# Performance work log

Hardware: AMD Instinct MI355X
Metric: run time of the kernel (lower is better)

Reference implementation:

```python
import jax, jax.numpy as jnp
import numpy as np

KS = 3           # deformable kernel size
N = KS * KS      # 9 sampling points
PAD = 1
STRIDE = 1


def conv2d(x, w, b=None, stride=1, padding=0):
    out = jax.lax.conv_general_dilated(
        x, w, (stride, stride), [(padding, padding), (padding, padding)],
        dimension_numbers=("NCHW", "OIHW", "NCHW"))
    if b is not None:
        out = out + b[None, :, None, None]
    return out


def setup_inputs() -> dict:
    key = jax.random.key(0)
    k0, k1, k2, k3 = jax.random.split(key, 4)
    B, C, H, W, OUTC = 2, 64, 128, 128, 64
    x = jax.random.normal(k0, (B, C, H, W), jnp.float32)
    # p_conv: Conv2d(C, 2*N, 3, padding=1); small weights so offsets are O(1)
    Wp = jax.random.normal(k1, (2 * N, C, 3, 3), jnp.float32) * 0.01
    bp = jax.random.normal(k2, (2 * N,), jnp.float32) * 0.1
    # final conv: Conv2d(C, OUTC, ks, stride=ks, bias=None) -> no bias
    Wc = jax.random.normal(k3, (OUTC, C, KS, KS), jnp.float32) / np.sqrt(C * KS * KS)
    return {"x": x, "Wp": Wp, "bp": bp, "Wc": Wc}


def _gather(x_pad, qx, qy):
    # x_pad: [b,c,Hp,Wp]; qx,qy: [b,h,w,N] int32 -> [b,c,h,w,N]
    b, c, Hp, Wpd = x_pad.shape
    _, h, w, n = qx.shape
    idx = (qx * Wpd + qy).reshape(b, 1, h * w * n)
    xf = x_pad.reshape(b, c, Hp * Wpd)
    g = jnp.take_along_axis(xf, jnp.broadcast_to(idx, (b, c, h * w * n)), axis=2)
    return g.reshape(b, c, h, w, n)


def reference(x, Wp, bp, Wc):
    b, c, h, w = x.shape
    dt = x.dtype
    offset = conv2d(x, Wp, bp, stride=STRIDE, padding=1)  # [b,2N,h,w]
    x_pad = jnp.pad(x, ((0, 0), (0, 0), (PAD, PAD), (PAD, PAD)))
    Hp, Wpd = x_pad.shape[2], x_pad.shape[3]

    # kernel-relative offsets p_n (x part first, then y part; n = kx*KS + ky)
    rng = jnp.arange(-(KS - 1) // 2, (KS - 1) // 2 + 1, dtype=dt)
    pnx, pny = jnp.meshgrid(rng, rng, indexing="ij")
    # base grid p_0 (starts at 1 because of the zero padding)
    p0x = jnp.arange(1, h * STRIDE + 1, STRIDE, dtype=dt)
    p0y = jnp.arange(1, w * STRIDE + 1, STRIDE, dtype=dt)

    # sampling locations, split into x/y coords: [b,h,w,N]
    px = offset[:, :N].transpose(0, 2, 3, 1) + pnx.ravel() + p0x[None, :, None, None]
    py = offset[:, N:].transpose(0, 2, 3, 1) + pny.ravel() + p0y[None, None, :, None]

    qltx = jnp.clip(jnp.floor(px), 0, Hp - 1).astype(jnp.int32)
    qlty = jnp.clip(jnp.floor(py), 0, Wpd - 1).astype(jnp.int32)
    qrbx = jnp.clip(jnp.floor(px) + 1, 0, Hp - 1).astype(jnp.int32)
    qrby = jnp.clip(jnp.floor(py) + 1, 0, Wpd - 1).astype(jnp.int32)

    px = jnp.clip(px, 0, Hp - 1)
    py = jnp.clip(py, 0, Wpd - 1)

    # bilinear weights
    g_lt = (1 + (qltx - px)) * (1 + (qlty - py))
    g_rb = (1 - (qrbx - px)) * (1 - (qrby - py))
    g_lb = (1 + (qltx - px)) * (1 - (qrby - py))
    g_rt = (1 - (qrbx - px)) * (1 + (qlty - py))

    x_lt = _gather(x_pad, qltx, qlty)
    x_rb = _gather(x_pad, qrbx, qrby)
    x_lb = _gather(x_pad, qltx, qrby)
    x_rt = _gather(x_pad, qrbx, qlty)

    x_off = (g_lt[:, None] * x_lt + g_rb[:, None] * x_rb
             + g_lb[:, None] * x_lb + g_rt[:, None] * x_rt)  # [b,c,h,w,N]

    # unfold N=(kx,ky) into spatial: [b,c,h*KS,w*KS]
    x_off = x_off.reshape(b, c, h, w, KS, KS).transpose(0, 1, 2, 4, 3, 5)
    x_off = x_off.reshape(b, c, h * KS, w * KS)

    return conv2d(x_off, Wc, None, stride=KS, padding=0)  # [b,outc,h,w]
```

## Files before the change

### kernel.cpp

```cpp
#include <hip/hip_runtime.h>
#include <hip/hip_bf16.h>

#define BB 2
#define CC 64
#define HH 128
#define WW 128
#define OC 64
#define HW (HH * WW)

typedef __attribute__((ext_vector_type(8))) short bf16x8;
typedef __attribute__((ext_vector_type(4))) float f32x4;

__device__ __forceinline__ unsigned short bfbits(float f) {
    __hip_bfloat16 h = __float2bfloat16(f);
    return __builtin_bit_cast(unsigned short, h);
}
__device__ __forceinline__ float frombits(unsigned short u) {
    unsigned int v = ((unsigned int)u) << 16;
    return __builtin_bit_cast(float, v);
}
__device__ __forceinline__ int iclamp(int v, int lo, int hi) {
    return v < lo ? lo : (v > hi ? hi : v);
}

#define WPK_OFF3    73728
#define XTB_OFF3    110592
#define WS3_NEED    4304896

__global__ __launch_bounds__(256) void kprep(
    const float* __restrict__ x,
    const float* __restrict__ Wc,
    const float* __restrict__ Wp,
    unsigned short* __restrict__ xTb,
    unsigned short* __restrict__ Wb3,
    unsigned short* __restrict__ wpk)
{
    __shared__ float tile[64 * 65];
    const int t  = threadIdx.x;
    const int bx = blockIdx.x;

    if (bx < 512) {
        const int b    = bx >> 8;
        const int pix0 = (bx & 255) * 64;
#pragma unroll
        for (int it = 0; it < 4; ++it) {
            const int item = it * 256 + t;
            const int c  = item & 63;
            const int p4 = item >> 6;
            const float4 v = *(const float4*)&x[(b * 64 + c) * 16384 + pix0 + p4 * 4];
            tile[(p4 * 4 + 0) * 65 + c] = v.x;
            tile[(p4 * 4 + 1) * 65 + c] = v.y;
            tile[(p4 * 4 + 2) * 65 + c] = v.z;
            tile[(p4 * 4 + 3) * 65 + c] = v.w;
        }
        __syncthreads();
#pragma unroll
        for (int it = 0; it < 4; ++it) {
            const int item = it * 256 + t;
            const int p  = item & 63;
            const int c4 = item >> 6;
            ushort4 v;
            v.x = bfbits(tile[p * 65 + c4 * 4 + 0]);
            v.y = bfbits(tile[p * 65 + c4 * 4 + 1]);
            v.z = bfbits(tile[p * 65 + c4 * 4 + 2]);
            v.w = bfbits(tile[p * 65 + c4 * 4 + 3]);
            *(ushort4*)&xTb[(b * 16384 + pix0 + p) * 64 + c4 * 4] = v;
        }
    } else if (bx < 656) {
        const int idx = (bx - 512) * 256 + t;
        if (idx < OC * 576) {
            const int j = idx & 7;
            const int r = (idx >> 3) & 15;
            const int m = (idx >> 7) & 3;
            const int a = idx >> 9;
            const int n = a >> 3;
            const int c = (a & 7) * 8 + j;
            const int oc = m * 16 + r;
            Wb3[idx] = bfbits(Wc[oc * 576 + c * 9 + n]);
        }
    } else {
        const int idx = (bx - 656) * 256 + t;
        if (idx < 32 * 576) {
            const int j = idx & 7;
            const int r = (idx >> 3) & 15;
            const int m = (idx >> 7) & 1;
            const int a = idx >> 8;
            const int n = a >> 3;
            const int c = (a & 7) * 8 + j;
            const int o = m * 16 + r;
            wpk[idx] = (o < 18) ? bfbits(Wp[o * 576 + c * 9 + n]) : (unsigned short)0;
        }
    }
}

__global__ __launch_bounds__(256, 2) void kmain(
    const unsigned short* __restrict__ xTb,
    const unsigned short* __restrict__ wpk,
    const unsigned short* __restrict__ Wb3,
    const float* __restrict__ bp,
    float* __restrict__ out)
{
    __shared__ __align__(16) unsigned short bbuf[72 * 256];
    __shared__ short   smi[288];
    __shared__ ushort4 smw[288];
    float* const odal = (float*)bbuf;

    const int t   = threadIdx.x;
    const int bxr = (blockIdx.x & 7) * 128 + (blockIdx.x >> 3);
    const int b   = bxr >> 9;
    const int i   = (bxr >> 2) & 127;
    const int j0  = (bxr & 3) << 5;
    const int l   = t & 63;
    const int w   = t >> 6;
    const int sh  = l >> 5;
    const int c0  = (l & 31) * 2;
    const unsigned short* xb = xTb + (((size_t)b) << 14) * 64;

#pragma unroll 6
    for (int q = 0; q < 36; ++q) {
        const int slot = w * 72 + q * 2 + sh;
        const int n   = slot >> 5;
        const int pos = slot & 31;
        const int kx = n / 3, ky = n - kx * 3;
        const int ii = i + kx - 1;
        const int jj = j0 + pos + ky - 1;
        const bool ok = ((unsigned)ii < (unsigned)HH) && ((unsigned)jj < (unsigned)WW);
        unsigned int v = 0;
        if (ok) v = *(const unsigned int*)&xb[(ii * WW + jj) * 64 + c0];
        const int row = n * 8 + (c0 >> 3);
        const int pc  = pos ^ (row & 7);
        *(unsigned int*)((char*)bbuf + row * 512 + pc * 16 + (c0 & 7) * 2) = v;
    }
    __syncthreads();

    {
        const int mt = w >> 1;
        const int pt = w & 1;
        const int r  = l & 15;
        const int kb = l >> 4;
        const unsigned short* wb = wpk + kb * 256 + mt * 128 + r * 8;
        f32x4 acc = {0.f, 0.f, 0.f, 0.f};
#pragma unroll 6
        for (int s = 0; s < 18; ++s) {
            const int a = s * 4 + kb;
            const bf16x8 af = *(const bf16x8*)(wb + s * 1024);
            const int pc = (pt * 16 + r) ^ (a & 7);
            const bf16x8 bf = *(const bf16x8*)&bbuf[a * 256 + pc * 8];
            acc = __builtin_amdgcn_mfma_f32_16x16x32_bf16(af, bf, acc, 0, 0, 0);
        }
        __syncthreads();
#pragma unroll
        for (int reg = 0; reg < 4; ++reg)
            odal[(mt * 16 + kb * 4 + reg) * 32 + pt * 16 + r] = acc[reg];
    }
    __syncthreads();

    {
        auto mkmeta = [&](int slot) {
            const int n   = slot >> 5;
            const int pos = slot & 31;
            const int kx  = n / 3, ky = n - kx * 3;
            const float offx = odal[n * 32 + pos] + bp[n];
            const float offy = odal[(9 + n) * 32 + pos] + bp[9 + n];
            const float px = offx + (float)(kx - 1) + (float)(i + 1);
            const float py = offy + (float)(ky - 1) + (float)(j0 + pos + 1);
            const float flx = floorf(px), fly = floorf(py);
            const float qltx = fminf(fmaxf(flx,       0.f), 129.f);
            const float qlty = fminf(fmaxf(fly,       0.f), 129.f);
            const float qrbx = fminf(fmaxf(flx + 1.f, 0.f), 129.f);
            const float qrby = fminf(fmaxf(fly + 1.f, 0.f), 129.f);
            const float pxc  = fminf(fmaxf(px, 0.f), 129.f);
            const float pyc  = fminf(fmaxf(py, 0.f), 129.f);
            const float gx0 = 1.f + (qltx - pxc), gx1 = 1.f - (qrbx - pxc);
            const float gy0 = 1.f + (qlty - pyc), gy1 = 1.f - (qrby - pyc);
            const int rx0 = (int)qltx - 1, rx1 = (int)qrbx - 1;
            const int ry0 = (int)qlty - 1, ry1 = (int)qrby - 1;
            const bool vx0 = (unsigned)rx0 < (unsigned)HH, vx1 = (unsigned)rx1 < (unsigned)HH;
            const bool vy0 = (unsigned)ry0 < (unsigned)WW, vy1 = (unsigned)ry1 < (unsigned)WW;
            const float w0 = (vx0 && vy0) ? gx0 * gy0 : 0.f;
            const float w1 = (vx1 && vy1) ? gx1 * gy1 : 0.f;
            const float w2 = (vx0 && vy1) ? gx0 * gy1 : 0.f;
            const float w3 = (vx1 && vy0) ? gx1 * gy0 : 0.f;
            smi[slot] = (short)(rx0 * WW + ry0);
            smw[slot] = make_ushort4(bfbits(w0), bfbits(w1), bfbits(w2), bfbits(w3));
        };
        mkmeta(t);
        if (t < 32) mkmeta(256 + t);
    }
    __syncthreads();

#pragma unroll 6
    for (int q = 0; q < 36; ++q) {
        const int slot = w * 72 + q * 2 + sh;
        const int n   = slot >> 5;
        const int pos = slot & 31;
        const int base = (int)smi[slot];
        const ushort4 wq = smw[slot];
        const float w0 = frombits(wq.x), w1 = frombits(wq.y);
        const float w2 = frombits(wq.z), w3 = frombits(wq.w);
        const int i0 = iclamp(base,       0, HW - 1);
        const int i1 = iclamp(base + 129, 0, HW - 1);
        const int i2 = iclamp(base + 1,   0, HW - 1);
        const int i3 = iclamp(base + 128, 0, HW - 1);
        const unsigned int u0 = *(const unsigned int*)&xb[i0 * 64 + c0];
        const unsigned int u1 = *(const unsigned int*)&xb[i1 * 64 + c0];
        const unsigned int u2 = *(const unsigned int*)&xb[i2 * 64 + c0];
        const unsigned int u3 = *(const unsigned int*)&xb[i3 * 64 + c0];
        float vlo = frombits((unsigned short)u0) * w0;
        vlo = fmaf(frombits((unsigned short)u1), w1, vlo);
        vlo = fmaf(frombits((unsigned short)u2), w2, vlo);
        vlo = fmaf(frombits((unsigned short)u3), w3, vlo);
        float vhi = frombits((unsigned short)(u0 >> 16)) * w0;
        vhi = fmaf(frombits((unsigned short)(u1 >> 16)), w1, vhi);
        vhi = fmaf(frombits((unsigned short)(u2 >> 16)), w2, vhi);
        vhi = fmaf(frombits((unsigned short)(u3 >> 16)), w3, vhi);
        const unsigned int vv = (unsigned int)bfbits(vlo)
                              | ((unsigned int)bfbits(vhi) << 16);
        const int row = n * 8 + (c0 >> 3);
        const int pc  = pos ^ (row & 7);
        *(unsigned int*)((char*)bbuf + row * 512 + pc * 16 + (c0 & 7) * 2) = vv;
    }
    __syncthreads();

    {
        const int r  = l & 15;
        const int kb = l >> 4;
        const unsigned short* wbase = Wb3 + kb * 512 + w * 128 + r * 8;
        f32x4 acc0 = {0.f, 0.f, 0.f, 0.f};
        f32x4 acc1 = {0.f, 0.f, 0.f, 0.f};
#pragma unroll 3
        for (int s = 0; s < 18; ++s) {
            const int a = s * 4 + kb;
            const bf16x8 af = *(const bf16x8*)(wbase + s * 2048);
            const int pc0 = (r ^ (a & 7));
            const bf16x8 bf0 = *(const bf16x8*)&bbuf[a * 256 + pc0 * 8];
            const bf16x8 bf1 = *(const bf16x8*)&bbuf[a * 256 + (16 + pc0) * 8];
            acc0 = __builtin_amdgcn_mfma_f32_16x16x32_bf16(af, bf0, acc0, 0, 0, 0);
            acc1 = __builtin_amdgcn_mfma_f32_16x16x32_bf16(af, bf1, acc1, 0, 0, 0);
        }
#pragma unroll
        for (int reg = 0; reg < 4; ++reg) {
            const int oc = w * 16 + kb * 4 + reg;
            float* o = out + ((b * OC + oc) * HH + i) * WW + j0;
            o[r]      = acc0[reg];
            o[16 + r] = acc1[reg];
        }
    }
}

__global__ __launch_bounds__(256) void wpack2fb(const float* __restrict__ Wc,
                                                unsigned short* __restrict__ Wb3)
{
    const int idx = blockIdx.x * 256 + threadIdx.x;
    if (idx < OC * 576) {
        const int j = idx & 7;
        const int r = (idx >> 3) & 15;
        const int m = (idx >> 7) & 3;
        const int a = idx >> 9;
        const int n = a >> 3;
        const int c = (a & 7) * 8 + j;
        const int oc = m * 16 + r;
        Wb3[idx] = bfbits(Wc[oc * 576 + c * 9 + n]);
    }
}

__global__ __launch_bounds__(256, 2) void dcn_wave(
    const float* __restrict__ x,
    const float* __restrict__ Wp,
    const float* __restrict__ bp,
    const unsigned short* __restrict__ Wb3,
    float* __restrict__ out)
{
    __shared__ __align__(16) unsigned char smraw[21312];
    float*          part = (float*)smraw;
    short*          mi   = (short*)(smraw + 18432);
    ushort4*        mw   = (ushort4*)(smraw + 19008);

    const int t   = threadIdx.x;
    const int bxr = (blockIdx.x & 7) * 128 + (blockIdx.x >> 3);
    const int b   = bxr >> 9;
    const int i   = (bxr >> 2) & 127;
    const int j0  = (bxr & 3) << 5;

    {
        const int grp = t >> 5;
        const int pp  = t & 31;
        const int j   = j0 + pp;
        float acc[18];
#pragma unroll
        for (int o = 0; o < 18; ++o) acc[o] = 0.f;
        const float* xg = x + (b * CC + grp * 8) * HW;
        for (int c = 0; c < 8; ++c) {
            float xv[9];
#pragma unroll
            for (int dx = 0; dx < 3; ++dx) {
                const int ii = i + dx - 1;
                const bool okx = (unsigned)ii < (unsigned)HH;
#pragma unroll
                for (int dy = 0; dy < 3; ++dy) {
                    const int jj = j + dy - 1;
                    const bool ok = okx && ((unsigned)jj < (unsigned)WW);
                    xv[dx * 3 + dy] = ok ? xg[c * HW + ii * WW + jj] : 0.f;
                }
            }
            const float* wp = Wp + (grp * 8 + c) * 9;
#pragma unroll
            for (int o = 0; o < 18; ++o) {
                const float* w = wp + o * 576;
#pragma unroll
                for (int k = 0; k < 9; ++k)
                    acc[o] = fmaf(xv[k], w[k], acc[o]);
            }
        }
#pragma unroll
        for (int o = 0; o < 18; ++o)
            part[grp * 576 + pp * 18 + o] = acc[o];
    }
    __syncthreads();

    {
        auto mkmeta = [&](int slot) {
            const int n   = slot >> 5;
            const int pos = slot & 31;
            const int kx  = n / 3, ky = n - kx * 3;
            float offx = bp[n], offy = bp[9 + n];
#pragma unroll
            for (int g = 0; g < 8; ++g) {
                offx += part[g * 576 + pos * 18 + n];
                offy += part[g * 576 + pos * 18 + 9 + n];
            }
            const float px = offx + (float)(kx - 1) + (float)(i + 1);
            const float py = offy + (float)(ky - 1) + (float)(j0 + pos + 1);
            const float flx = floorf(px), fly = floorf(py);
            const float qltx = fminf(fmaxf(flx,       0.f), 129.f);
            const float qlty = fminf(fmaxf(fly,       0.f), 129.f);
            const float qrbx = fminf(fmaxf(flx + 1.f, 0.f), 129.f);
            const float qrby = fminf(fmaxf(fly + 1.f, 0.f), 129.f);
            const float pxc  = fminf(fmaxf(px, 0.f), 129.f);
            const float pyc  = fminf(fmaxf(py, 0.f), 129.f);
            const float gx0 = 1.f + (qltx - pxc), gx1 = 1.f - (qrbx - pxc);
            const float gy0 = 1.f + (qlty - pyc), gy1 = 1.f - (qrby - pyc);
            const int rx0 = (int)qltx - 1, rx1 = (int)qrbx - 1;
            const int ry0 = (int)qlty - 1, ry1 = (int)qrby - 1;
            const bool vx0 = (unsigned)rx0 < (unsigned)HH, vx1 = (unsigned)rx1 < (unsigned)HH;
            const bool vy0 = (unsigned)ry0 < (unsigned)WW, vy1 = (unsigned)ry1 < (unsigned)WW;
            const float w0 = (vx0 && vy0) ? gx0 * gy0 : 0.f;
            const float w1 = (vx1 && vy1) ? gx1 * gy1 : 0.f;
            const float w2 = (vx0 && vy1) ? gx0 * gy1 : 0.f;
            const float w3 = (vx1 && vy0) ? gx1 * gy0 : 0.f;
            mi[slot] = (short)(rx0 * WW + ry0);
            mw[slot] = make_ushort4(bfbits(w0), bfbits(w1), bfbits(w2), bfbits(w3));
        };
        mkmeta(t);
        if (t < 32) mkmeta(256 + t);
    }
    __syncthreads();

    const int l    = t & 63;
    const int w_   = t >> 6;
    const int sw   = w_ >> 1;
    const int half = w_ & 1;
    const int r    = l & 15;
    const int kb   = l >> 4;
    const int posl = sw * 16 + r;
    const float* xb = x + b * (CC * HW);
    const unsigned short* wbase = Wb3 + (half * 36 + kb) * 512 + r * 8;

    f32x4 acc0 = {0.f, 0.f, 0.f, 0.f};
    f32x4 acc1 = {0.f, 0.f, 0.f, 0.f};
    f32x4 acc2 = {0.f, 0.f, 0.f, 0.f};
    f32x4 acc3 = {0.f, 0.f, 0.f, 0.f};

#pragma unroll 3
    for (int s = 0; s < 9; ++s) {
        const int a  = half * 36 + s * 4 + kb;
        const int n  = a >> 3;
        const int c0 = (a & 7) * 8;
        const int slot = n * 32 + posl;
        const int base = (int)mi[slot];
        const ushort4 wq = mw[slot];
        const float w0 = frombits(wq.x), w1 = frombits(wq.y);
        const float w2 = frombits(wq.z), w3 = frombits(wq.w);
        const int i0 = iclamp(base,       0, HW - 1);
        const int i1 = iclamp(base + 129, 0, HW - 1);
        const int i2 = iclamp(base + 1,   0, HW - 1);
        const int i3 = iclamp(base + 128, 0, HW - 1);
        const float* p = xb + c0 * HW;
        bf16x8 bfrag;
#pragma unroll
        for (int j = 0; j < 8; ++j) {
            float v = p[i0] * w0;
            v = fmaf(p[i1], w1, v);
            v = fmaf(p[i2], w2, v);
            v = fmaf(p[i3], w3, v);
            bfrag[j] = (short)bfbits(v);
            p += HW;
        }
        const unsigned short* wp8 = wbase + s * 2048;
        const bf16x8 af0 = *(const bf16x8*)(wp8);
        const bf16x8 af1 = *(const bf16x8*)(wp8 + 128);
        const bf16x8 af2 = *(const bf16x8*)(wp8 + 256);
        const bf16x8 af3 = *(const bf16x8*)(wp8 + 384);
        acc0 = __builtin_amdgcn_mfma_f32_16x16x32_bf16(af0, bfrag, acc0, 0, 0, 0);
        acc1 = __builtin_amdgcn_mfma_f32_16x16x32_bf16(af1, bfrag, acc1, 0, 0, 0);
        acc2 = __builtin_amdgcn_mfma_f32_16x16x32_bf16(af2, bfrag, acc2, 0, 0, 0);
        acc3 = __builtin_amdgcn_mfma_f32_16x16x32_bf16(af3, bfrag, acc3, 0, 0, 0);
    }

    float* red = part;
    if (half) {
        *(f32x4*)&red[sw * 1024 + 0 * 256 + l * 4] = acc0;
        *(f32x4*)&red[sw * 1024 + 1 * 256 + l * 4] = acc1;
        *(f32x4*)&red[sw * 1024 + 2 * 256 + l * 4] = acc2;
        *(f32x4*)&red[sw * 1024 + 3 * 256 + l * 4] = acc3;
    }
    __syncthreads();
    if (!half) {
        acc0 += *(const f32x4*)&red[sw * 1024 + 0 * 256 + l * 4];
        acc1 += *(const f32x4*)&red[sw * 1024 + 1 * 256 + l * 4];
        acc2 += *(const f32x4*)&red[sw * 1024 + 2 * 256 + l * 4];
        acc3 += *(const f32x4*)&red[sw * 1024 + 3 * 256 + l * 4];
        const int jcol = j0 + posl;
        f32x4 av[4] = {acc0, acc1, acc2, acc3};
#pragma unroll
        for (int m = 0; m < 4; ++m)
#pragma unroll
            for (int reg = 0; reg < 4; ++reg) {
                const int oc = m * 16 + kb * 4 + reg;
                out[((b * OC + oc) * HH + i) * WW + jcol] = av[m][reg];
            }
    }
}

extern "C" void kernel_launch(void* const* d_in, const int* in_sizes, int n_in,
                              void* d_out, int out_size, void* d_ws, size_t ws_size,
                              hipStream_t stream) {
    const float* x  = (const float*)d_in[0];
    const float* Wp = (const float*)d_in[1];
    const float* bp = (const float*)d_in[2];
    const float* Wc = (const float*)d_in[3];
    float* out = (float*)d_out;
    unsigned char* ws = (unsigned char*)d_ws;
    unsigned short* Wb3 = (unsigned short*)ws;

    if (ws_size >= (size_t)WS3_NEED) {
        unsigned short* wpk = (unsigned short*)(ws + WPK_OFF3);
        unsigned short* xTb = (unsigned short*)(ws + XTB_OFF3);
        kprep<<<dim3(728), dim3(256), 0, stream>>>(x, Wc, Wp, xTb, Wb3, wpk);
        kmain<<<dim3(BB * HH * 4), dim3(256), 0, stream>>>(xTb, wpk, Wb3, bp, out);
    } else {
        wpack2fb<<<dim3((OC * 576 + 255) / 256), dim3(256), 0, stream>>>(Wc, Wb3);
        dcn_wave<<<dim3(BB * HH * 4), dim3(256), 0, stream>>>(x, Wp, bp, Wb3, out);
    }
}
```

Measured before the change: 40.73 us.

## Fuse prep and main kernels into one cooperative launch with grid sync

Merges the preparation kernel (bf16 transpose of x and weight packing) and the main deformable-conv kernel into a single cooperative kernel separated by a grid-wide barrier. The goal is to drop the second kernel launch and the gap between the two kernels. It adds host-side occupancy queries on every call plus the cost of a grid sync, and it falls back to two launches when all 1024 blocks cannot be co-resident. The old fallback path for a small workspace is removed, so the workspace is now assumed to be large enough.

Measured after the change: 38.39 us. -5.7%, faster.

```diff
diff --git a/kernel.cpp b/kernel.cpp
--- a/kernel.cpp
+++ b/kernel.cpp
@@ -1,5 +1,8 @@
 #include <hip/hip_runtime.h>
 #include <hip/hip_bf16.h>
+#include <hip/hip_cooperative_groups.h>
+
+namespace cg = cooperative_groups;
 
 #define BB 2
 #define CC 64
@@ -27,18 +30,14 @@
 #define XTB_OFF3    110592
 #define WS3_NEED    4304896
 
-__global__ __launch_bounds__(256) void kprep(
-    const float* __restrict__ x,
-    const float* __restrict__ Wc,
+
+__device__ __forceinline__ void prep_section(
+    int bx, int t, float* tile,
+    const float* __restrict__ x, const float* __restrict__ Wc,
     const float* __restrict__ Wp,
-    unsigned short* __restrict__ xTb,
-    unsigned short* __restrict__ Wb3,
+    unsigned short* __restrict__ xTb, unsigned short* __restrict__ Wb3,
     unsigned short* __restrict__ wpk)
 {
-    __shared__ float tile[64 * 65];
-    const int t  = threadIdx.x;
-    const int bx = blockIdx.x;
-
     if (bx < 512) {
         const int b    = bx >> 8;
         const int pix0 = (bx & 255) * 64;
@@ -78,7 +77,7 @@
             const int oc = m * 16 + r;
             Wb3[idx] = bfbits(Wc[oc * 576 + c * 9 + n]);
         }
-    } else {
+    } else if (bx < 728) {
         const int idx = (bx - 656) * 256 + t;
         if (idx < 32 * 576) {
             const int j = idx & 7;
@@ -93,20 +92,20 @@
     }
 }
 
-__global__ __launch_bounds__(256, 2) void kmain(
+__device__ __forceinline__ void main_section(
+    int bxl, int t, unsigned char* smem,
     const unsigned short* __restrict__ xTb,
     const unsigned short* __restrict__ wpk,
     const unsigned short* __restrict__ Wb3,
     const float* __restrict__ bp,
     float* __restrict__ out)
 {
-    __shared__ __align__(16) unsigned short bbuf[72 * 256];
-    __shared__ short   smi[288];
-    __shared__ ushort4 smw[288];
-    float* const odal = (float*)bbuf;
-
-    const int t   = threadIdx.x;
-    const int bxr = (blockIdx.x & 7) * 128 + (blockIdx.x >> 3);
+    unsigned short* bbuf = (unsigned short*)smem;
+    short*   smi = (short*)(smem + 36864);
+    ushort4* smw = (ushort4*)(smem + 37440);
+    float* const odal = (float*)smem;
+
+    const int bxr = (bxl & 7) * 128 + (bxl >> 3);
     const int b   = bxr >> 9;
     const int i   = (bxr >> 2) & 127;
     const int j0  = (bxr & 3) << 5;
@@ -248,188 +247,49 @@
     }
 }
 
-__global__ __launch_bounds__(256) void wpack2fb(const float* __restrict__ Wc,
-                                                unsigned short* __restrict__ Wb3)
-{
-    const int idx = blockIdx.x * 256 + threadIdx.x;
-    if (idx < OC * 576) {
-        const int j = idx & 7;
-        const int r = (idx >> 3) & 15;
-        const int m = (idx >> 7) & 3;
-        const int a = idx >> 9;
-        const int n = a >> 3;
-        const int c = (a & 7) * 8 + j;
-        const int oc = m * 16 + r;
-        Wb3[idx] = bfbits(Wc[oc * 576 + c * 9 + n]);
-    }
-}
-
-__global__ __launch_bounds__(256, 2) void dcn_wave(
+__global__ __launch_bounds__(256, 2) void kfused(
     const float* __restrict__ x,
+    const float* __restrict__ Wc,
     const float* __restrict__ Wp,
     const float* __restrict__ bp,
+    unsigned short* __restrict__ xTb,
+    unsigned short* __restrict__ Wb3,
+    unsigned short* __restrict__ wpk,
+    float* __restrict__ out)
+{
+    __shared__ __align__(16) unsigned char smem[39744];
+    const int t  = threadIdx.x;
+    const int bx = blockIdx.x;
+
+    prep_section(bx, t, (float*)smem, x, Wc, Wp, xTb, Wb3, wpk);
+
+    __threadfence();
+    cg::this_grid().sync();
+
+    main_section(bx, t, smem, xTb, wpk, Wb3, bp, out);
+}
+
+__global__ __launch_bounds__(256) void kprep(
+    const float* __restrict__ x,
+    const float* __restrict__ Wc,
+    const float* __restrict__ Wp,
+    unsigned short* __restrict__ xTb,
+    unsigned short* __restrict__ Wb3,
+    unsigned short* __restrict__ wpk)
+{
+    __shared__ float tile[64 * 65];
+    prep_section(blockIdx.x, threadIdx.x, tile, x, Wc, Wp, xTb, Wb3, wpk);
+}
+
+__global__ __launch_bounds__(256, 2) void kmain(
+    const unsigned short* __restrict__ xTb,
+    const unsigned short* __restrict__ wpk,
     const unsigned short* __restrict__ Wb3,
+    const float* __restrict__ bp,
     float* __restrict__ out)
 {
-    __shared__ __align__(16) unsigned char smraw[21312];
-    float*          part = (float*)smraw;
-    short*          mi   = (short*)(smraw + 18432);
-    ushort4*        mw   = (ushort4*)(smraw + 19008);
-
-    const int t   = threadIdx.x;
-    const int bxr = (blockIdx.x & 7) * 128 + (blockIdx.x >> 3);
-    const int b   = bxr >> 9;
-    const int i   = (bxr >> 2) & 127;
-    const int j0  = (bxr & 3) << 5;
-
-    {
-        const int grp = t >> 5;
-        const int pp  = t & 31;
-        const int j   = j0 + pp;
-        float acc[18];
-#pragma unroll
-        for (int o = 0; o < 18; ++o) acc[o] = 0.f;
-        const float* xg = x + (b * CC + grp * 8) * HW;
-        for (int c = 0; c < 8; ++c) {
-            float xv[9];
-#pragma unroll
-            for (int dx = 0; dx < 3; ++dx) {
-                const int ii = i + dx - 1;
-                const bool okx = (unsigned)ii < (unsigned)HH;
-#pragma unroll
-                for (int dy = 0; dy < 3; ++dy) {
-                    const int jj = j + dy - 1;
-                    const bool ok = okx && ((unsigned)jj < (unsigned)WW);
-                    xv[dx * 3 + dy] = ok ? xg[c * HW + ii * WW + jj] : 0.f;
-                }
-            }
-            const float* wp = Wp + (grp * 8 + c) * 9;
-#pragma unroll
-            for (int o = 0; o < 18; ++o) {
-                const float* w = wp + o * 576;
-#pragma unroll
-                for (int k = 0; k < 9; ++k)
-                    acc[o] = fmaf(xv[k], w[k], acc[o]);
-            }
-        }
-#pragma unroll
-        for (int o = 0; o < 18; ++o)
-            part[grp * 576 + pp * 18 + o] = acc[o];
-    }
-    __syncthreads();
-
-    {
-        auto mkmeta = [&](int slot) {
-            const int n   = slot >> 5;
-            const int pos = slot & 31;
-            const int kx  = n / 3, ky = n - kx * 3;
-            float offx = bp[n], offy = bp[9 + n];
-#pragma unroll
-            for (int g = 0; g < 8; ++g) {
-                offx += part[g * 576 + pos * 18 + n];
-                offy += part[g * 576 + pos * 18 + 9 + n];
-            }
-            const float px = offx + (float)(kx - 1) + (float)(i + 1);
-            const float py = offy + (float)(ky - 1) + (float)(j0 + pos + 1);
-            const float flx = floorf(px), fly = floorf(py);
-            const float qltx = fminf(fmaxf(flx,       0.f), 129.f);
-            const float qlty = fminf(fmaxf(fly,       0.f), 129.f);
-            const float qrbx = fminf(fmaxf(flx + 1.f, 0.f), 129.f);
-            const float qrby = fminf(fmaxf(fly + 1.f, 0.f), 129.f);
-            const float pxc  = fminf(fmaxf(px, 0.f), 129.f);
-            const float pyc  = fminf(fmaxf(py, 0.f), 129.f);
-            const float gx0 = 1.f + (qltx - pxc), gx1 = 1.f - (qrbx - pxc);
-            const float gy0 = 1.f + (qlty - pyc), gy1 = 1.f - (qrby - pyc);
-            const int rx0 = (int)qltx - 1, rx1 = (int)qrbx - 1;
-            const int ry0 = (int)qlty - 1, ry1 = (int)qrby - 1;
-            const bool vx0 = (unsigned)rx0 < (unsigned)HH, vx1 = (unsigned)rx1 < (unsigned)HH;
-            const bool vy0 = (unsigned)ry0 < (unsigned)WW, vy1 = (unsigned)ry1 < (unsigned)WW;
-            const float w0 = (vx0 && vy0) ? gx0 * gy0 : 0.f;
-            const float w1 = (vx1 && vy1) ? gx1 * gy1 : 0.f;
-            const float w2 = (vx0 && vy1) ? gx0 * gy1 : 0.f;
-            const float w3 = (vx1 && vy0) ? gx1 * gy0 : 0.f;
-            mi[slot] = (short)(rx0 * WW + ry0);
-            mw[slot] = make_ushort4(bfbits(w0), bfbits(w1), bfbits(w2), bfbits(w3));
-        };
-        mkmeta(t);
-        if (t < 32) mkmeta(256 + t);
-    }
-    __syncthreads();
-
-    const int l    = t & 63;
-    const int w_   = t >> 6;
-    const int sw   = w_ >> 1;
-    const int half = w_ & 1;
-    const int r    = l & 15;
-    const int kb   = l >> 4;
-    const int posl = sw * 16 + r;
-    const float* xb = x + b * (CC * HW);
-    const unsigned short* wbase = Wb3 + (half * 36 + kb) * 512 + r * 8;
-
-    f32x4 acc0 = {0.f, 0.f, 0.f, 0.f};
-    f32x4 acc1 = {0.f, 0.f, 0.f, 0.f};
-    f32x4 acc2 = {0.f, 0.f, 0.f, 0.f};
-    f32x4 acc3 = {0.f, 0.f, 0.f, 0.f};
-
-#pragma unroll 3
-    for (int s = 0; s < 9; ++s) {
-        const int a  = half * 36 + s * 4 + kb;
-        const int n  = a >> 3;
-        const int c0 = (a & 7) * 8;
-        const int slot = n * 32 + posl;
-        const int base = (int)mi[slot];
-        const ushort4 wq = mw[slot];
-        const float w0 = frombits(wq.x), w1 = frombits(wq.y);
-        const float w2 = frombits(wq.z), w3 = frombits(wq.w);
-        const int i0 = iclamp(base,       0, HW - 1);
-        const int i1 = iclamp(base + 129, 0, HW - 1);
-        const int i2 = iclamp(base + 1,   0, HW - 1);
-        const int i3 = iclamp(base + 128, 0, HW - 1);
-        const float* p = xb + c0 * HW;
-        bf16x8 bfrag;
-#pragma unroll
-        for (int j = 0; j < 8; ++j) {
-            float v = p[i0] * w0;
-            v = fmaf(p[i1], w1, v);
-            v = fmaf(p[i2], w2, v);
-            v = fmaf(p[i3], w3, v);
-            bfrag[j] = (short)bfbits(v);
-            p += HW;
-        }
-        const unsigned short* wp8 = wbase + s * 2048;
-        const bf16x8 af0 = *(const bf16x8*)(wp8);
-        const bf16x8 af1 = *(const bf16x8*)(wp8 + 128);
-        const bf16x8 af2 = *(const bf16x8*)(wp8 + 256);
-        const bf16x8 af3 = *(const bf16x8*)(wp8 + 384);
-        acc0 = __builtin_amdgcn_mfma_f32_16x16x32_bf16(af0, bfrag, acc0, 0, 0, 0);
-        acc1 = __builtin_amdgcn_mfma_f32_16x16x32_bf16(af1, bfrag, acc1, 0, 0, 0);
-        acc2 = __builtin_amdgcn_mfma_f32_16x16x32_bf16(af2, bfrag, acc2, 0, 0, 0);
-        acc3 = __builtin_amdgcn_mfma_f32_16x16x32_bf16(af3, bfrag, acc3, 0, 0, 0);
-    }
-
-    float* red = part;
-    if (half) {
-        *(f32x4*)&red[sw * 1024 + 0 * 256 + l * 4] = acc0;
-        *(f32x4*)&red[sw * 1024 + 1 * 256 + l * 4] = acc1;
-        *(f32x4*)&red[sw * 1024 + 2 * 256 + l * 4] = acc2;
-        *(f32x4*)&red[sw * 1024 + 3 * 256 + l * 4] = acc3;
-    }
-    __syncthreads();
-    if (!half) {
-        acc0 += *(const f32x4*)&red[sw * 1024 + 0 * 256 + l * 4];
-        acc1 += *(const f32x4*)&red[sw * 1024 + 1 * 256 + l * 4];
-        acc2 += *(const f32x4*)&red[sw * 1024 + 2 * 256 + l * 4];
-        acc3 += *(const f32x4*)&red[sw * 1024 + 3 * 256 + l * 4];
-        const int jcol = j0 + posl;
-        f32x4 av[4] = {acc0, acc1, acc2, acc3};
-#pragma unroll
-        for (int m = 0; m < 4; ++m)
-#pragma unroll
-            for (int reg = 0; reg < 4; ++reg) {
-                const int oc = m * 16 + kb * 4 + reg;
-                out[((b * OC + oc) * HH + i) * WW + jcol] = av[m][reg];
-            }
-    }
+    __shared__ __align__(16) unsigned char smem[39744];
+    main_section(blockIdx.x, threadIdx.x, smem, xTb, wpk, Wb3, bp, out);
 }
 
 extern "C" void kernel_launch(void* const* d_in, const int* in_sizes, int n_in,
@@ -442,14 +302,23 @@
     float* out = (float*)d_out;
     unsigned char* ws = (unsigned char*)d_ws;
     unsigned short* Wb3 = (unsigned short*)ws;
-
-    if (ws_size >= (size_t)WS3_NEED) {
-        unsigned short* wpk = (unsigned short*)(ws + WPK_OFF3);
-        unsigned short* xTb = (unsigned short*)(ws + XTB_OFF3);
-        kprep<<<dim3(728), dim3(256), 0, stream>>>(x, Wc, Wp, xTb, Wb3, wpk);
-        kmain<<<dim3(BB * HH * 4), dim3(256), 0, stream>>>(xTb, wpk, Wb3, bp, out);
-    } else {
-        wpack2fb<<<dim3((OC * 576 + 255) / 256), dim3(256), 0, stream>>>(Wc, Wb3);
-        dcn_wave<<<dim3(BB * HH * 4), dim3(256), 0, stream>>>(x, Wp, bp, Wb3, out);
-    }
-}
+    unsigned short* wpk = (unsigned short*)(ws + WPK_OFF3);
+    unsigned short* xTb = (unsigned short*)(ws + XTB_OFF3);
+
+    int maxb = 0, ncu = 0, dev = 0;
+    hipGetDevice(&dev);
+    hipDeviceGetAttribute(&ncu, hipDeviceAttributeMultiprocessorCount, dev);
+    hipOccupancyMaxActiveBlocksPerMultiprocessor(&maxb, (const void*)kfused, 256, 0);
+    bool coop = ((long)maxb * ncu >= BB * HH * 4);
+
+    if (coop) {
+        void* args[] = {(void*)&x, (void*)&Wc, (void*)&Wp, (void*)&bp,
+                        (void*)&xTb, (void*)&Wb3, (void*)&wpk, (void*)&out};
+        hipError_t e = hipLaunchCooperativeKernel((const void*)kfused,
+                                                  dim3(BB * HH * 4), dim3(256),
+                                                  args, 0, stream);
+        if (e == hipSuccess) return;
+    }
+    kprep<<<dim3(728), dim3(256), 0, stream>>>(x, Wc, Wp, xTb, Wb3, wpk);
+    kmain<<<dim3(BB * HH * 4), dim3(256), 0, stream>>>(xTb, wpk, Wb3, bp, out);
+}
```
